# Kernel optimization log

Measured on AMD Instinct MI355X. Metric: run time of the kernel, lower is better.

The kernel has to match this reference:

```python
import jax, jax.numpy as jnp
import numpy as np

ASIZE, VSIZE, HSIZE, MSIZE = 128, 512, 512, 48


def _xavier(key, shape):
    fan_in, fan_out = shape[1], shape[0]
    limit = float(np.sqrt(6.0 / (fan_in + fan_out)))
    return jax.random.uniform(key, shape, jnp.float32, -limit, limit)


def setup_inputs() -> dict:
    key = jax.random.key(0)
    ks = jax.random.split(key, 9)
    B, T = 32, 64
    audio = jax.random.normal(ks[0], (B, T, ASIZE), jnp.float32)
    video = jax.random.normal(ks[1], (B, T, MSIZE, VSIZE), jnp.float32)
    return {
        "audio": audio,
        "video": video,
        "W_audio": _xavier(ks[2], (HSIZE, ASIZE)),
        "b_audio": jnp.zeros((HSIZE,), jnp.float32),
        "W_video": _xavier(ks[3], (HSIZE, VSIZE)),
        "b_video": jnp.zeros((HSIZE,), jnp.float32),
        "W_v": _xavier(ks[4], (MSIZE, HSIZE)),
        "W_g": _xavier(ks[5], (MSIZE, HSIZE)),
        "W_h": _xavier(ks[6], (1, MSIZE)),
    }


def reference(audio, video, W_audio, b_audio, W_video, b_video, W_v, W_g, W_h):
    B, T, N, vsize = video.shape  # N == MSIZE == 48 required by the broadcast
    V = video.reshape(B * T, N, vsize)                      # [BT, N, vsize]
    v = jax.nn.relu(jnp.einsum('bnv,hv->bnh', V, W_video) + b_video)  # [BT,N,h]
    a = jax.nn.relu(audio.reshape(-1, audio.shape[-1]) @ W_audio.T + b_audio)  # [BT,h]
    inter = a @ W_g.T                                        # [BT, m]
    # torch broadcast: [BT,N,m] + [BT,m,1] with N==m -> inter indexed by spatial pos
    content = jnp.einsum('bnh,mh->bnm', v, W_v) + inter[:, :, None]
    z = jnp.einsum('bnm,om->bno', jnp.tanh(content), W_h)[..., 0]  # [BT, N]
    alpha = jax.nn.softmax(z, axis=-1)                        # [BT, N]
    c = jnp.einsum('bn,bnv->bv', alpha, V)                    # [BT, vsize]
    return c.reshape(B, T, vsize)
```

## Files before the change

### kernel.cpp

```cpp
#include <hip/hip_runtime.h>
#include <hip/hip_bf16.h>

typedef __bf16 bf16x8 __attribute__((ext_vector_type(8)));
typedef __bf16 bf16x4 __attribute__((ext_vector_type(4)));
typedef float  f32x4  __attribute__((ext_vector_type(4)));

#define BT    2048
#define MDIM  48

#define WS_WVID  0
#define WS_WV    (512*512*2)
#define WS_WG    (WS_WV + 48*512*2)
#define WS_INTER (WS_WG + 48*512*2)

__global__ __launch_bounds__(256) void convert_weights(
    const float* __restrict__ Wvid, const float* __restrict__ Wv,
    const float* __restrict__ Wg,
    __bf16* __restrict__ wvid_k, __bf16* __restrict__ wv_b,
    __bf16* __restrict__ wg_b) {
    int i = blockIdx.x * blockDim.x + threadIdx.x;
    const int nv = 65536, n2 = 6144;
    if (i < nv) {
        int h = i >> 7, k4 = i & 127;
        float4 f = ((const float4*)Wvid)[i];
        bf16x4 o = {(__bf16)f.x, (__bf16)f.y, (__bf16)f.z, (__bf16)f.w};
        *(bf16x4*)(wvid_k + (size_t)(((k4 >> 1) * 512 + h) * 8 + (k4 & 1) * 4)) = o;
    } else if (i < nv + n2) {
        int j = i - nv;
        float4 f = ((const float4*)Wv)[j];
        bf16x4 o = {(__bf16)f.x, (__bf16)f.y, (__bf16)f.z, (__bf16)f.w};
        ((bf16x4*)wv_b)[j] = o;
    } else {
        int j = i - nv - n2;
        float4 f = ((const float4*)Wg)[j];
        bf16x4 o = {(__bf16)f.x, (__bf16)f.y, (__bf16)f.z, (__bf16)f.w};
        ((bf16x4*)wg_b)[j] = o;
    }
}

__global__ __launch_bounds__(512) void audio_batch(
    const float* __restrict__ audio, const float* __restrict__ Wa,
    const float* __restrict__ ba, const __bf16* __restrict__ wg_b,
    float* __restrict__ inter) {
    __shared__ float  ain[16 * 128];
    __shared__ __bf16 as_s[64 * 17 * 8];

    const int bt0 = blockIdx.x * 16;
    const int t   = threadIdx.x;

    ((float4*)ain)[t] = ((const float4*)(audio + (size_t)bt0 * 128))[t];
    __syncthreads();

    float acc[16];
    float bias = ba[t];
    #pragma unroll
    for (int b = 0; b < 16; ++b) acc[b] = bias;
    const float4* wr = (const float4*)(Wa + (size_t)t * 128);
    #pragma unroll 4
    for (int k4 = 0; k4 < 32; ++k4) {
        float4 wv = wr[k4];
        #pragma unroll
        for (int b = 0; b < 16; ++b) {
            float4 av = ((const float4*)ain)[b * 32 + k4];
            acc[b] += av.x*wv.x + av.y*wv.y + av.z*wv.z + av.w*wv.w;
        }
    }
    #pragma unroll
    for (int b = 0; b < 16; ++b)
        as_s[(((t >> 3) * 17 + b) << 3) | (t & 7)] = (__bf16)fmaxf(acc[b], 0.f);
    __syncthreads();

    const int w = t >> 6, lane = t & 63, l16 = lane & 15, quad = lane >> 4;
    if (w < 3) {
        f32x4 c = {0.f, 0.f, 0.f, 0.f};
        const __bf16* bp = wg_b + (size_t)(w * 16 + l16) * 512 + quad * 8;
        const __bf16* ap = &as_s[((quad * 17 + l16)) * 8];
        bf16x8 aC = *(const bf16x8*)ap;
        bf16x8 bC = *(const bf16x8*)bp;
        #pragma unroll
        for (int kt = 0; kt < 16; ++kt) {
            bf16x8 aN, bN;
            if (kt < 15) {
                aN = *(const bf16x8*)(ap + (kt + 1) * (4 * 17 * 8));
                bN = *(const bf16x8*)(bp + (kt + 1) * 32);
            }
            c = __builtin_amdgcn_mfma_f32_16x16x32_bf16(aC, bC, c, 0, 0, 0);
            if (kt < 15) { aC = aN; bC = bN; }
        }
        #pragma unroll
        for (int r = 0; r < 4; ++r)
            inter[(size_t)(bt0 + quad * 4 + r) * 48 + w * 16 + l16] = c[r];
    }
}

__global__ __launch_bounds__(256, 1) void main_fused(
    const float* __restrict__ video, const float* __restrict__ bvid,
    const __bf16* __restrict__ wvid_k, const __bf16* __restrict__ wv_b,
    const float* __restrict__ Wh, const float* __restrict__ inter_g,
    float* __restrict__ out) {

    __shared__ uint4 pool4[3136];
    __shared__ float inter_s[MDIM];
    __shared__ float z_s[MDIM];
    __shared__ float alpha_s[MDIM];
    __shared__ float content8[256];

    char* pool = (char*)pool4;

    const int bt   = blockIdx.x;
    const int tid  = threadIdx.x;
    const int w    = tid >> 6;
    const int lane = tid & 63;
    const int l16  = lane & 15;
    const int quad = lane >> 4;

    const float* Vg = video + (size_t)bt * (48 * 512);
    const char*  bbase = (const char*)wvid_k;

    if (tid < MDIM) { inter_s[tid] = inter_g[bt * MDIM + tid]; z_s[tid] = 0.f; }
    content8[tid] = 0.f;

    const int kcl = tid & 15;
    const int s_b = tid >> 4;

    #pragma unroll
    for (int m = 0; m < 3; ++m) {
        const int s = s_b + m * 16;
        const float4* p = (const float4*)(Vg + s * 512 + kcl * 8);
        float4 x = p[0], y = p[1];
        bf16x8 g = {(__bf16)x.x, (__bf16)x.y, (__bf16)x.z, (__bf16)x.w,
                    (__bf16)y.x, (__bf16)y.y, (__bf16)y.z, (__bf16)y.w};
        *(bf16x8*)(pool + (kcl * 49 + s) * 16) = g;
    }

    const int bIdx0 = quad * 8192 + (w * 128 + l16) * 16;

    f32x4 acc[3][8];
    #pragma unroll
    for (int mt = 0; mt < 3; ++mt)
        #pragma unroll
        for (int j = 0; j < 8; ++j) {
            f32x4 z = {0.f, 0.f, 0.f, 0.f};
            acc[mt][j] = z;
        }

    __syncthreads();

    #pragma unroll
    for (int c = 0; c < 4; ++c) {
        float4 px[3], py[3];
        if (c < 3) {
            #pragma unroll
            for (int m = 0; m < 3; ++m) {
                const int s  = s_b + m * 16;
                const int kc = (c + 1) * 16 + kcl;
                const float4* p = (const float4*)(Vg + s * 512 + kc * 8);
                px[m] = p[0]; py[m] = p[1];
            }
        }
        #pragma unroll
        for (int k = 0; k < 4; ++k) {
            const int kt = c * 4 + k;
            bf16x8 a[3];
            #pragma unroll
            for (int mt = 0; mt < 3; ++mt)
                a[mt] = *(const bf16x8*)(pool + ((4 * kt + quad) * 49 + mt * 16 + l16) * 16);
            bf16x8 b[8];
            #pragma unroll
            for (int j = 0; j < 8; ++j)
                b[j] = *(const bf16x8*)(bbase + bIdx0 + kt * 32768 + j * 256);
            #pragma unroll
            for (int mt = 0; mt < 3; ++mt)
                #pragma unroll
                for (int j = 0; j < 8; ++j)
                    acc[mt][j] = __builtin_amdgcn_mfma_f32_16x16x32_bf16(
                                     a[mt], b[j], acc[mt][j], 0, 0, 0);
        }
        if (c < 3) {
            #pragma unroll
            for (int m = 0; m < 3; ++m) {
                const int s  = s_b + m * 16;
                const int kc = (c + 1) * 16 + kcl;
                bf16x8 g = {(__bf16)px[m].x, (__bf16)px[m].y, (__bf16)px[m].z, (__bf16)px[m].w,
                            (__bf16)py[m].x, (__bf16)py[m].y, (__bf16)py[m].z, (__bf16)py[m].w};
                *(bf16x8*)(pool + (kc * 49 + s) * 16) = g;
            }
        }
        __syncthreads();
    }

    #pragma unroll
    for (int j = 0; j < 8; ++j) {
        const int h = w * 128 + j * 16 + l16;
        float bias = bvid[h];
        #pragma unroll
        for (int mt = 0; mt < 3; ++mt) {
            #pragma unroll
            for (int r = 0; r < 4; ++r) {
                const int s = mt * 16 + quad * 4 + r;
                *(__bf16*)(pool + s * 1040 + h * 2) =
                    (__bf16)fmaxf(acc[mt][j][r] + bias, 0.f);
            }
        }
    }
    __syncthreads();

    {
        #pragma unroll
        for (int half = 0; half < 2; ++half) {
            const int T  = w + half * 4;
            const int ti = T / 3, tj = T - ti * 3;
            const __bf16* bp = wv_b + (size_t)(tj * 16 + l16) * 512 + quad * 8;
            const char*   ap = pool + (ti * 16 + l16) * 1040 + quad * 16;
            f32x4 c3e = {0.f, 0.f, 0.f, 0.f};
            f32x4 c3o = {0.f, 0.f, 0.f, 0.f};
            #pragma unroll
            for (int kt = 0; kt < 16; kt += 2) {
                bf16x8 a0 = *(const bf16x8*)(ap + kt * 64);
                bf16x8 b0 = *(const bf16x8*)(bp + kt * 32);
                c3e = __builtin_amdgcn_mfma_f32_16x16x32_bf16(a0, b0, c3e, 0, 0, 0);
                bf16x8 a1 = *(const bf16x8*)(ap + (kt + 1) * 64);
                bf16x8 b1 = *(const bf16x8*)(bp + (kt + 1) * 32);
                c3o = __builtin_amdgcn_mfma_f32_16x16x32_bf16(a1, b1, c3o, 0, 0, 0);
            }
            f32x4 c3 = c3e + c3o;
            float wh = Wh[tj * 16 + l16];
            #pragma unroll
            for (int r = 0; r < 4; ++r) {
                const int s = ti * 16 + quad * 4 + r;
                float contrib = tanhf(c3[r] + inter_s[s]) * wh;
                contrib += __shfl_xor(contrib, 1);
                contrib += __shfl_xor(contrib, 2);
                contrib += __shfl_xor(contrib, 4);
                contrib += __shfl_xor(contrib, 8);
                if (l16 == 0) atomicAdd(&z_s[s], contrib);
            }
        }
        f32x4 p8 = {0.f, 0.f, 0.f, 0.f};
        #pragma unroll
        for (int q = 0; q < 4; ++q) {
            const int kt = 4 * w + q;
            bf16x8 a8 = *(const bf16x8*)(pool + (32 + l16) * 1040 + kt * 64 + quad * 16);
            bf16x8 b8 = *(const bf16x8*)(wv_b + (size_t)(32 + l16) * 512 + kt * 32 + quad * 8);
            p8 = __builtin_amdgcn_mfma_f32_16x16x32_bf16(a8, b8, p8, 0, 0, 0);
        }
        #pragma unroll
        for (int r = 0; r < 4; ++r)
            atomicAdd(&content8[(quad * 4 + r) * 16 + l16], p8[r]);
    }
    __syncthreads();

    if (w == 0) {
        float wh = Wh[32 + l16];
        #pragma unroll
        for (int r = 0; r < 4; ++r) {
            const int s = 32 + quad * 4 + r;
            float contrib = tanhf(content8[(quad * 4 + r) * 16 + l16] + inter_s[s]) * wh;
            contrib += __shfl_xor(contrib, 1);
            contrib += __shfl_xor(contrib, 2);
            contrib += __shfl_xor(contrib, 4);
            contrib += __shfl_xor(contrib, 8);
            if (l16 == 0) atomicAdd(&z_s[s], contrib);
        }
    }
    __syncthreads();

    if (w == 0) {
        float x = (lane < MDIM) ? z_s[lane] : -INFINITY;
        float mx = x;
        #pragma unroll
        for (int off = 32; off >= 1; off >>= 1) mx = fmaxf(mx, __shfl_xor(mx, off));
        float e = (lane < MDIM) ? expf(x - mx) : 0.f;
        float sm = e;
        #pragma unroll
        for (int off = 32; off >= 1; off >>= 1) sm += __shfl_xor(sm, off);
        if (lane < MDIM) alpha_s[lane] = e / sm;
    }
    __syncthreads();

    float a5 = 0.f, b5 = 0.f;
    #pragma unroll
    for (int s = 0; s < MDIM; ++s) {
        const float al = alpha_s[s];
        a5 += al * Vg[s * 512 + tid];
        b5 += al * Vg[s * 512 + 256 + tid];
    }
    out[(size_t)bt * 512 + tid]       = a5;
    out[(size_t)bt * 512 + 256 + tid] = b5;
}

extern "C" void kernel_launch(void* const* d_in, const int* in_sizes, int n_in,
                              void* d_out, int out_size, void* d_ws, size_t ws_size,
                              hipStream_t stream) {
    const float* audio   = (const float*)d_in[0];
    const float* video   = (const float*)d_in[1];
    const float* W_audio = (const float*)d_in[2];
    const float* b_audio = (const float*)d_in[3];
    const float* W_video = (const float*)d_in[4];
    const float* b_video = (const float*)d_in[5];
    const float* W_v     = (const float*)d_in[6];
    const float* W_g     = (const float*)d_in[7];
    const float* W_h     = (const float*)d_in[8];
    float* out = (float*)d_out;

    char* ws = (char*)d_ws;
    __bf16* wvid_k = (__bf16*)(ws + WS_WVID);
    __bf16* wv_b   = (__bf16*)(ws + WS_WV);
    __bf16* wg_b   = (__bf16*)(ws + WS_WG);
    float*  inter  = (float*)(ws + WS_INTER);

    convert_weights<<<304, 256, 0, stream>>>(W_video, W_v, W_g, wvid_k, wv_b, wg_b);
    audio_batch<<<BT / 16, 512, 0, stream>>>(audio, W_audio, b_audio, wg_b, inter);
    main_fused<<<BT, 256, 0, stream>>>(video, b_video, wvid_k, wv_b, W_h, inter, out);
}
```

Measured before the change: 400.5 us.

## Software-pipeline B-operand loads across MFMA steps and interleave content tiles

The main GEMM loop now double-buffers the weight B fragments in registers. Step kt+1's B loads are issued before step kt's MFMAs, and a sched_barrier keeps the compiler from reordering them. The next video chunk's global loads move after the chunk's MFMAs. The content GEMM now runs both tiles together with register-prefetched A/B operands, which interleaves two independent MFMA chains. The goal is to hide global and LDS load latency behind matrix math, at the cost of more VGPR pressure that could lower occupancy or cause spills.

```diff
diff --git a/kernel.cpp b/kernel.cpp
--- a/kernel.cpp
+++ b/kernel.cpp
@@ -135,6 +135,11 @@
 
     const int bIdx0 = quad * 8192 + (w * 128 + l16) * 16;
 
+    bf16x8 bC[8];
+    #pragma unroll
+    for (int j = 0; j < 8; ++j)
+        bC[j] = *(const bf16x8*)(bbase + bIdx0 + j * 256);
+
     f32x4 acc[3][8];
     #pragma unroll
     for (int mt = 0; mt < 3; ++mt)
@@ -148,8 +153,33 @@
 
     #pragma unroll
     for (int c = 0; c < 4; ++c) {
-        float4 px[3], py[3];
+        #pragma unroll
+        for (int k = 0; k < 4; ++k) {
+            const int kt = c * 4 + k;
+            bf16x8 a[3];
+            #pragma unroll
+            for (int mt = 0; mt < 3; ++mt)
+                a[mt] = *(const bf16x8*)(pool + ((4 * kt + quad) * 49 + mt * 16 + l16) * 16);
+            bf16x8 bN[8];
+            if (kt < 15) {
+                #pragma unroll
+                for (int j = 0; j < 8; ++j)
+                    bN[j] = *(const bf16x8*)(bbase + bIdx0 + (kt + 1) * 32768 + j * 256);
+            }
+            __builtin_amdgcn_sched_barrier(0);
+            #pragma unroll
+            for (int mt = 0; mt < 3; ++mt)
+                #pragma unroll
+                for (int j = 0; j < 8; ++j)
+                    acc[mt][j] = __builtin_amdgcn_mfma_f32_16x16x32_bf16(
+                                     a[mt], bC[j], acc[mt][j], 0, 0, 0);
+            if (kt < 15) {
+                #pragma unroll
+                for (int j = 0; j < 8; ++j) bC[j] = bN[j];
+            }
+        }
         if (c < 3) {
+            float4 px[3], py[3];
             #pragma unroll
             for (int m = 0; m < 3; ++m) {
                 const int s  = s_b + m * 16;
@@ -157,26 +187,6 @@
                 const float4* p = (const float4*)(Vg + s * 512 + kc * 8);
                 px[m] = p[0]; py[m] = p[1];
             }
-        }
-        #pragma unroll
-        for (int k = 0; k < 4; ++k) {
-            const int kt = c * 4 + k;
-            bf16x8 a[3];
-            #pragma unroll
-            for (int mt = 0; mt < 3; ++mt)
-                a[mt] = *(const bf16x8*)(pool + ((4 * kt + quad) * 49 + mt * 16 + l16) * 16);
-            bf16x8 b[8];
-            #pragma unroll
-            for (int j = 0; j < 8; ++j)
-                b[j] = *(const bf16x8*)(bbase + bIdx0 + kt * 32768 + j * 256);
-            #pragma unroll
-            for (int mt = 0; mt < 3; ++mt)
-                #pragma unroll
-                for (int j = 0; j < 8; ++j)
-                    acc[mt][j] = __builtin_amdgcn_mfma_f32_16x16x32_bf16(
-                                     a[mt], b[j], acc[mt][j], 0, 0, 0);
-        }
-        if (c < 3) {
             #pragma unroll
             for (int m = 0; m < 3; ++m) {
                 const int s  = s_b + m * 16;
@@ -206,35 +216,54 @@
     __syncthreads();
 
     {
-        #pragma unroll
-        for (int half = 0; half < 2; ++half) {
-            const int T  = w + half * 4;
-            const int ti = T / 3, tj = T - ti * 3;
-            const __bf16* bp = wv_b + (size_t)(tj * 16 + l16) * 512 + quad * 8;
-            const char*   ap = pool + (ti * 16 + l16) * 1040 + quad * 16;
-            f32x4 c3e = {0.f, 0.f, 0.f, 0.f};
-            f32x4 c3o = {0.f, 0.f, 0.f, 0.f};
-            #pragma unroll
-            for (int kt = 0; kt < 16; kt += 2) {
-                bf16x8 a0 = *(const bf16x8*)(ap + kt * 64);
-                bf16x8 b0 = *(const bf16x8*)(bp + kt * 32);
-                c3e = __builtin_amdgcn_mfma_f32_16x16x32_bf16(a0, b0, c3e, 0, 0, 0);
-                bf16x8 a1 = *(const bf16x8*)(ap + (kt + 1) * 64);
-                bf16x8 b1 = *(const bf16x8*)(bp + (kt + 1) * 32);
-                c3o = __builtin_amdgcn_mfma_f32_16x16x32_bf16(a1, b1, c3o, 0, 0, 0);
-            }
-            f32x4 c3 = c3e + c3o;
-            float wh = Wh[tj * 16 + l16];
-            #pragma unroll
-            for (int r = 0; r < 4; ++r) {
-                const int s = ti * 16 + quad * 4 + r;
-                float contrib = tanhf(c3[r] + inter_s[s]) * wh;
-                contrib += __shfl_xor(contrib, 1);
-                contrib += __shfl_xor(contrib, 2);
-                contrib += __shfl_xor(contrib, 4);
-                contrib += __shfl_xor(contrib, 8);
-                if (l16 == 0) atomicAdd(&z_s[s], contrib);
-            }
+        const int TA = w,  TB = w + 4;
+        const int tiA = TA / 3, tjA = TA - tiA * 3;
+        const int tiB = TB / 3, tjB = TB - tiB * 3;
+        const __bf16* bpA = wv_b + (size_t)(tjA * 16 + l16) * 512 + quad * 8;
+        const __bf16* bpB = wv_b + (size_t)(tjB * 16 + l16) * 512 + quad * 8;
+        const char*   apA = pool + (tiA * 16 + l16) * 1040 + quad * 16;
+        const char*   apB = pool + (tiB * 16 + l16) * 1040 + quad * 16;
+        f32x4 cA = {0.f, 0.f, 0.f, 0.f};
+        f32x4 cB = {0.f, 0.f, 0.f, 0.f};
+        bf16x8 aA = *(const bf16x8*)apA;
+        bf16x8 aB = *(const bf16x8*)apB;
+        bf16x8 bA = *(const bf16x8*)bpA;
+        bf16x8 bB = *(const bf16x8*)bpB;
+        #pragma unroll
+        for (int kt = 0; kt < 16; ++kt) {
+            bf16x8 aAn, aBn, bAn, bBn;
+            if (kt < 15) {
+                aAn = *(const bf16x8*)(apA + (kt + 1) * 64);
+                aBn = *(const bf16x8*)(apB + (kt + 1) * 64);
+                bAn = *(const bf16x8*)(bpA + (kt + 1) * 32);
+                bBn = *(const bf16x8*)(bpB + (kt + 1) * 32);
+            }
+            __builtin_amdgcn_sched_barrier(0);
+            cA = __builtin_amdgcn_mfma_f32_16x16x32_bf16(aA, bA, cA, 0, 0, 0);
+            cB = __builtin_amdgcn_mfma_f32_16x16x32_bf16(aB, bB, cB, 0, 0, 0);
+            if (kt < 15) { aA = aAn; aB = aBn; bA = bAn; bB = bBn; }
+        }
+        float whA = Wh[tjA * 16 + l16];
+        float whB = Wh[tjB * 16 + l16];
+        #pragma unroll
+        for (int r = 0; r < 4; ++r) {
+            const int sA = tiA * 16 + quad * 4 + r;
+            float contrib = tanhf(cA[r] + inter_s[sA]) * whA;
+            contrib += __shfl_xor(contrib, 1);
+            contrib += __shfl_xor(contrib, 2);
+            contrib += __shfl_xor(contrib, 4);
+            contrib += __shfl_xor(contrib, 8);
+            if (l16 == 0) atomicAdd(&z_s[sA], contrib);
+        }
+        #pragma unroll
+        for (int r = 0; r < 4; ++r) {
+            const int sB = tiB * 16 + quad * 4 + r;
+            float contrib = tanhf(cB[r] + inter_s[sB]) * whB;
+            contrib += __shfl_xor(contrib, 1);
+            contrib += __shfl_xor(contrib, 2);
+            contrib += __shfl_xor(contrib, 4);
+            contrib += __shfl_xor(contrib, 8);
+            if (l16 == 0) atomicAdd(&z_s[sB], contrib);
         }
         f32x4 p8 = {0.f, 0.f, 0.f, 0.f};
         #pragma unroll
```

Measured after the change: 387.3 us. 1.03x faster.

## Halve LDS footprint, double-buffer video staging, fuse second GEMM per warp

Applied to the files above, without the earlier changes.

Shrinks the shared-memory pool by double-buffering only one 16-chunk of the video tile instead of staging the whole bf16 slab, and raises launch bounds to allow two blocks per CU. Weight B-fragments are prefetched one k-step ahead with a sched_barrier so loads overlap MFMAs. The content GEMM is restructured so each warp multiplies its own 128-wide h slice against W_v through a swizzled per-warp scratch, accumulating partial results into a shared content matrix with atomics. The tanh/Wh reduction is then done in one pass over the content matrix. This trades more LDS atomics and register pressure under a tighter occupancy bound for better latency hiding.

```diff
diff --git a/kernel.cpp b/kernel.cpp
--- a/kernel.cpp
+++ b/kernel.cpp
@@ -93,17 +93,17 @@
     }
 }
 
-__global__ __launch_bounds__(256, 1) void main_fused(
+__global__ __launch_bounds__(256, 2) void main_fused(
     const float* __restrict__ video, const float* __restrict__ bvid,
     const __bf16* __restrict__ wvid_k, const __bf16* __restrict__ wv_b,
     const float* __restrict__ Wh, const float* __restrict__ inter_g,
     float* __restrict__ out) {
 
-    __shared__ uint4 pool4[3136];
+    __shared__ uint4 pool4[1568];
+    __shared__ float content_s[48 * 49];
     __shared__ float inter_s[MDIM];
     __shared__ float z_s[MDIM];
     __shared__ float alpha_s[MDIM];
-    __shared__ float content8[256];
 
     char* pool = (char*)pool4;
 
@@ -117,8 +117,9 @@
     const float* Vg = video + (size_t)bt * (48 * 512);
     const char*  bbase = (const char*)wvid_k;
 
-    if (tid < MDIM) { inter_s[tid] = inter_g[bt * MDIM + tid]; z_s[tid] = 0.f; }
-    content8[tid] = 0.f;
+    if (tid < MDIM) inter_s[tid] = inter_g[bt * MDIM + tid];
+    #pragma unroll
+    for (int i = tid; i < 48 * 49; i += 256) content_s[i] = 0.f;
 
     const int kcl = tid & 15;
     const int s_b = tid >> 4;
@@ -135,6 +136,11 @@
 
     const int bIdx0 = quad * 8192 + (w * 128 + l16) * 16;
 
+    bf16x8 bC[8];
+    #pragma unroll
+    for (int j = 0; j < 8; ++j)
+        bC[j] = *(const bf16x8*)(bbase + bIdx0 + j * 256);
+
     f32x4 acc[3][8];
     #pragma unroll
     for (int mt = 0; mt < 3; ++mt)
@@ -148,120 +154,108 @@
 
     #pragma unroll
     for (int c = 0; c < 4; ++c) {
-        float4 px[3], py[3];
-        if (c < 3) {
-            #pragma unroll
-            for (int m = 0; m < 3; ++m) {
-                const int s  = s_b + m * 16;
-                const int kc = (c + 1) * 16 + kcl;
-                const float4* p = (const float4*)(Vg + s * 512 + kc * 8);
-                px[m] = p[0]; py[m] = p[1];
-            }
-        }
+        const int rbuf = (c & 1) * 12544;
         #pragma unroll
         for (int k = 0; k < 4; ++k) {
             const int kt = c * 4 + k;
             bf16x8 a[3];
             #pragma unroll
             for (int mt = 0; mt < 3; ++mt)
-                a[mt] = *(const bf16x8*)(pool + ((4 * kt + quad) * 49 + mt * 16 + l16) * 16);
-            bf16x8 b[8];
-            #pragma unroll
-            for (int j = 0; j < 8; ++j)
-                b[j] = *(const bf16x8*)(bbase + bIdx0 + kt * 32768 + j * 256);
+                a[mt] = *(const bf16x8*)(pool + rbuf +
+                            ((4 * k + quad) * 49 + mt * 16 + l16) * 16);
+            bf16x8 bN[8];
+            if (kt < 15) {
+                #pragma unroll
+                for (int j = 0; j < 8; ++j)
+                    bN[j] = *(const bf16x8*)(bbase + bIdx0 + (kt + 1) * 32768 + j * 256);
+            }
+            __builtin_amdgcn_sched_barrier(0);
             #pragma unroll
             for (int mt = 0; mt < 3; ++mt)
                 #pragma unroll
                 for (int j = 0; j < 8; ++j)
                     acc[mt][j] = __builtin_amdgcn_mfma_f32_16x16x32_bf16(
-                                     a[mt], b[j], acc[mt][j], 0, 0, 0);
+                                     a[mt], bC[j], acc[mt][j], 0, 0, 0);
+            if (kt < 15) {
+                #pragma unroll
+                for (int j = 0; j < 8; ++j) bC[j] = bN[j];
+            }
         }
         if (c < 3) {
+            const int wbuf = ((c + 1) & 1) * 12544;
+            float4 px[3], py[3];
             #pragma unroll
             for (int m = 0; m < 3; ++m) {
-                const int s  = s_b + m * 16;
-                const int kc = (c + 1) * 16 + kcl;
+                const int s = s_b + m * 16;
+                const float4* p = (const float4*)(Vg + s * 512 + ((c + 1) * 16 + kcl) * 8);
+                px[m] = p[0]; py[m] = p[1];
+            }
+            #pragma unroll
+            for (int m = 0; m < 3; ++m) {
+                const int s = s_b + m * 16;
                 bf16x8 g = {(__bf16)px[m].x, (__bf16)px[m].y, (__bf16)px[m].z, (__bf16)px[m].w,
                             (__bf16)py[m].x, (__bf16)py[m].y, (__bf16)py[m].z, (__bf16)py[m].w};
-                *(bf16x8*)(pool + (kc * 49 + s) * 16) = g;
+                *(bf16x8*)(pool + wbuf + (kcl * 49 + s) * 16) = g;
             }
         }
         __syncthreads();
     }
 
-    #pragma unroll
-    for (int j = 0; j < 8; ++j) {
-        const int h = w * 128 + j * 16 + l16;
-        float bias = bvid[h];
+    {
+        char* scr = pool + w * 4096;
+        float bias_j[8];
+        #pragma unroll
+        for (int j = 0; j < 8; ++j) bias_j[j] = bvid[w * 128 + j * 16 + l16];
+
         #pragma unroll
         for (int mt = 0; mt < 3; ++mt) {
             #pragma unroll
-            for (int r = 0; r < 4; ++r) {
-                const int s = mt * 16 + quad * 4 + r;
-                *(__bf16*)(pool + s * 1040 + h * 2) =
-                    (__bf16)fmaxf(acc[mt][j][r] + bias, 0.f);
-            }
-        }
-    }
-    __syncthreads();
-
-    {
-        #pragma unroll
-        for (int half = 0; half < 2; ++half) {
-            const int T  = w + half * 4;
-            const int ti = T / 3, tj = T - ti * 3;
-            const __bf16* bp = wv_b + (size_t)(tj * 16 + l16) * 512 + quad * 8;
-            const char*   ap = pool + (ti * 16 + l16) * 1040 + quad * 16;
-            f32x4 c3e = {0.f, 0.f, 0.f, 0.f};
-            f32x4 c3o = {0.f, 0.f, 0.f, 0.f};
-            #pragma unroll
-            for (int kt = 0; kt < 16; kt += 2) {
-                bf16x8 a0 = *(const bf16x8*)(ap + kt * 64);
-                bf16x8 b0 = *(const bf16x8*)(bp + kt * 32);
-                c3e = __builtin_amdgcn_mfma_f32_16x16x32_bf16(a0, b0, c3e, 0, 0, 0);
-                bf16x8 a1 = *(const bf16x8*)(ap + (kt + 1) * 64);
-                bf16x8 b1 = *(const bf16x8*)(bp + (kt + 1) * 32);
-                c3o = __builtin_amdgcn_mfma_f32_16x16x32_bf16(a1, b1, c3o, 0, 0, 0);
-            }
-            f32x4 c3 = c3e + c3o;
-            float wh = Wh[tj * 16 + l16];
-            #pragma unroll
-            for (int r = 0; r < 4; ++r) {
-                const int s = ti * 16 + quad * 4 + r;
-                float contrib = tanhf(c3[r] + inter_s[s]) * wh;
-                contrib += __shfl_xor(contrib, 1);
-                contrib += __shfl_xor(contrib, 2);
-                contrib += __shfl_xor(contrib, 4);
-                contrib += __shfl_xor(contrib, 8);
-                if (l16 == 0) atomicAdd(&z_s[s], contrib);
-            }
-        }
-        f32x4 p8 = {0.f, 0.f, 0.f, 0.f};
-        #pragma unroll
-        for (int q = 0; q < 4; ++q) {
-            const int kt = 4 * w + q;
-            bf16x8 a8 = *(const bf16x8*)(pool + (32 + l16) * 1040 + kt * 64 + quad * 16);
-            bf16x8 b8 = *(const bf16x8*)(wv_b + (size_t)(32 + l16) * 512 + kt * 32 + quad * 8);
-            p8 = __builtin_amdgcn_mfma_f32_16x16x32_bf16(a8, b8, p8, 0, 0, 0);
-        }
-        #pragma unroll
-        for (int r = 0; r < 4; ++r)
-            atomicAdd(&content8[(quad * 4 + r) * 16 + l16], p8[r]);
-    }
-    __syncthreads();
-
-    if (w == 0) {
-        float wh = Wh[32 + l16];
-        #pragma unroll
-        for (int r = 0; r < 4; ++r) {
-            const int s = 32 + quad * 4 + r;
-            float contrib = tanhf(content8[(quad * 4 + r) * 16 + l16] + inter_s[s]) * wh;
-            contrib += __shfl_xor(contrib, 1);
-            contrib += __shfl_xor(contrib, 2);
-            contrib += __shfl_xor(contrib, 4);
-            contrib += __shfl_xor(contrib, 8);
-            if (l16 == 0) atomicAdd(&z_s[s], contrib);
-        }
+            for (int j = 0; j < 8; ++j) {
+                #pragma unroll
+                for (int r = 0; r < 4; ++r) {
+                    const int sp = quad * 4 + r;
+                    const int h2 = (j * 16 + l16) * 2;
+                    *(__bf16*)(scr + sp * 256 + (h2 ^ ((sp & 7) << 5))) =
+                        (__bf16)fmaxf(acc[mt][j][r] + bias_j[j], 0.f);
+                }
+            }
+            f32x4 cc[3];
+            #pragma unroll
+            for (int nt = 0; nt < 3; ++nt) { f32x4 z = {0.f,0.f,0.f,0.f}; cc[nt] = z; }
+            #pragma unroll
+            for (int ks = 0; ks < 4; ++ks) {
+                bf16x8 pa = *(const bf16x8*)(scr + l16 * 256 +
+                                ((ks * 64 + quad * 16) ^ ((l16 & 7) << 5)));
+                #pragma unroll
+                for (int nt = 0; nt < 3; ++nt) {
+                    bf16x8 pb = *(const bf16x8*)(wv_b + (size_t)(nt * 16 + l16) * 512 +
+                                                 w * 128 + ks * 32 + quad * 8);
+                    cc[nt] = __builtin_amdgcn_mfma_f32_16x16x32_bf16(pa, pb, cc[nt], 0, 0, 0);
+                }
+            }
+            #pragma unroll
+            for (int nt = 0; nt < 3; ++nt)
+                #pragma unroll
+                for (int r = 0; r < 4; ++r)
+                    atomicAdd(&content_s[(mt * 16 + quad * 4 + r) * 49 + nt * 16 + l16],
+                              cc[nt][r]);
+        }
+    }
+    __syncthreads();
+
+    if (w < 3) {
+        const int s = 16 * w + (lane >> 2);
+        const int q = lane & 3;
+        const float ins = inter_s[s];
+        float zp = 0.f;
+        #pragma unroll
+        for (int mm = 0; mm < 12; ++mm) {
+            const int m = q * 12 + mm;
+            zp += tanhf(content_s[s * 49 + m] + ins) * Wh[m];
+        }
+        zp += __shfl_xor(zp, 1);
+        zp += __shfl_xor(zp, 2);
+        if (q == 0) z_s[s] = zp;
     }
     __syncthreads();
 
```

Result: slower. 455.7 us (+13.8%).
